# Performance work log

Hardware: AMD Instinct MI355X
Metric: run time of the kernel (lower is better)

The kernel has to match this reference:

```python
import jax, jax.numpy as jnp
import numpy as np

N_NODES = 100000
N_EDGES = 3200000
N_F = 128
HIDDEN = 128
N_PRED = 8
K_HOPS = 3
N_GRAPHS = 64


def setup_inputs() -> dict:
    key = jax.random.key(0)
    k1, k2, k3, k4, k5, k6, k7, k8 = jax.random.split(key, 8)
    x = jax.random.normal(k1, (N_NODES, N_F), dtype=jnp.float32)
    edge_index = jax.random.randint(k2, (2, N_EDGES), 0, N_NODES, dtype=jnp.int64)
    edge_attr = jax.random.uniform(k3, (N_EDGES,), dtype=jnp.float32)
    batch = jnp.sort(jax.random.randint(k4, (N_NODES,), 0, N_GRAPHS, dtype=jnp.int64))
    # SGConv internal Linear: in=n_f, out=hidden (applied after K propagations)
    s1 = 1.0 / np.sqrt(N_F)
    W_conv = jax.random.uniform(k5, (HIDDEN, N_F), dtype=jnp.float32, minval=-s1, maxval=s1)
    b_conv = jax.random.uniform(k6, (HIDDEN,), dtype=jnp.float32, minval=-s1, maxval=s1)
    s2 = 1.0 / np.sqrt(HIDDEN)
    W_lin = jax.random.uniform(k7, (N_PRED, HIDDEN), dtype=jnp.float32, minval=-s2, maxval=s2)
    b_lin = jax.random.uniform(k8, (N_PRED,), dtype=jnp.float32, minval=-s2, maxval=s2)
    return {"x": x, "edge_index": edge_index, "edge_attr": edge_attr, "batch": batch,
            "W_conv": W_conv, "b_conv": b_conv, "W_lin": W_lin, "b_lin": b_lin}


def _gcn_norm(edge_index, edge_weight, num_nodes):
    # Add self-loops with weight 1 (PyG gcn_norm default), then symmetric normalize.
    loop = jnp.arange(num_nodes, dtype=edge_index.dtype)
    row = jnp.concatenate([edge_index[0], loop])
    col = jnp.concatenate([edge_index[1], loop])
    w = jnp.concatenate([edge_weight, jnp.ones((num_nodes,), dtype=edge_weight.dtype)])
    deg = jax.ops.segment_sum(w, col, num_segments=num_nodes)
    dinv = jnp.where(deg > 0, jax.lax.rsqrt(jnp.where(deg > 0, deg, 1.0)), 0.0)
    norm = dinv[row] * w * dinv[col]
    return row, col, norm


def reference(x, edge_index, edge_attr, batch, W_conv, b_conv, W_lin, b_lin):
    N = x.shape[0]
    row, col, norm = _gcn_norm(edge_index, edge_attr, N)
    h = x
    for _ in range(K_HOPS):  # K repeated gather-scale-scatter propagations
        h = jax.ops.segment_sum(norm[:, None] * h[row], col, num_segments=N)
    h = h @ W_conv.T + b_conv  # SGConv linear: [N, hidden]
    # global_mean_pool by batch id
    sums = jax.ops.segment_sum(h, batch, num_segments=N_GRAPHS)
    cnt = jax.ops.segment_sum(jnp.ones((N,), dtype=h.dtype), batch, num_segments=N_GRAPHS)
    pooled = sums / jnp.maximum(cnt, 1.0)[:, None]
    # dropout(p=0.5) is identity in eval mode
    return pooled @ W_lin.T + b_lin
```

## Files before the change

kernel.cpp:

```cpp
#include <hip/hip_runtime.h>

#define NN 100000
#define NE 3200000
#define NF 128
#define NH 128
#define NP 8
#define NG 64

#define CS 16000
#define NC 7
#define NW 64
#define ES (NE / NW)

#define PT 64
#define GP 1024

#define SCAN_B 1024
#define SCAN_NBLK 98

__device__ __forceinline__ unsigned short f2bf(float f) {
    unsigned u = __float_as_uint(f);
    return (unsigned short)((u + 0x7fffu + ((u >> 16) & 1u)) >> 16);
}
__device__ __forceinline__ float bf2f(unsigned short b) {
    return __uint_as_float((unsigned)b << 16);
}

__global__ void k_init(float* __restrict__ cnt, float* __restrict__ psum) {
    int i = blockIdx.x * blockDim.x + threadIdx.x;
    if (i < NG) cnt[i] = 0.0f;
    if (i < NG * NH) psum[i] = 0.0f;
}

__global__ __launch_bounds__(256) void k_hist(const int* __restrict__ row,
                                              unsigned* __restrict__ H) {
    __shared__ unsigned hist[CS];
    int w = blockIdx.x % NW, c = blockIdx.x / NW;
    int rbase = c * CS;
    int nb = (rbase + CS <= NN) ? CS : (NN - rbase);
    for (int i = threadIdx.x; i < nb; i += 256) hist[i] = 0u;
    __syncthreads();
    const int4* r4 = (const int4*)(row + (size_t)w * ES);
    for (int i = threadIdx.x; i < ES / 8; i += 256) {
        int4 a = r4[2 * i], b = r4[2 * i + 1];
        int rs[8] = {a.x, a.y, a.z, a.w, b.x, b.y, b.z, b.w};
#pragma unroll
        for (int j = 0; j < 8; ++j) {
            unsigned rr = (unsigned)(rs[j] - rbase);
            if (rr < (unsigned)nb) atomicAdd(&hist[rr], 1u);
        }
    }
    __syncthreads();
    for (int i = threadIdx.x; i < nb; i += 256) H[(size_t)w * NN + rbase + i] = hist[i];
}

__global__ __launch_bounds__(256) void k_deg_hist(const int* __restrict__ col,
                                                  const float* __restrict__ wt,
                                                  float* __restrict__ Hd) {
    __shared__ float dh[CS];
    int w = blockIdx.x % NW, c = blockIdx.x / NW;
    int rbase = c * CS;
    int nb = (rbase + CS <= NN) ? CS : (NN - rbase);
    for (int i = threadIdx.x; i < nb; i += 256) dh[i] = 0.0f;
    __syncthreads();
    const int4*   c4 = (const int4*)(col + (size_t)w * ES);
    const float4* w4 = (const float4*)(wt + (size_t)w * ES);
    for (int i = threadIdx.x; i < ES / 8; i += 256) {
        int4 a = c4[2 * i], b = c4[2 * i + 1];
        float4 wa = w4[2 * i], wb = w4[2 * i + 1];
        int cc[8] = {a.x, a.y, a.z, a.w, b.x, b.y, b.z, b.w};
        float ww[8] = {wa.x, wa.y, wa.z, wa.w, wb.x, wb.y, wb.z, wb.w};
#pragma unroll
        for (int j = 0; j < 8; ++j) {
            unsigned rr = (unsigned)(cc[j] - rbase);
            if (rr < (unsigned)nb) atomicAdd(&dh[rr], ww[j]);
        }
    }
    __syncthreads();
    for (int i = threadIdx.x; i < nb; i += 256) Hd[(size_t)w * NN + rbase + i] = dh[i];
}

__global__ void k_cnt(const int* __restrict__ batch, float* __restrict__ cnt) {
    __shared__ float c[NG];
    int t = threadIdx.x;
    if (t < NG) c[t] = 0.0f;
    __syncthreads();
    int i = blockIdx.x * blockDim.x + t;
    if (i < NN) atomicAdd(&c[batch[i]], 1.0f);
    __syncthreads();
    if (t < NG && c[t] != 0.0f) atomicAdd(&cnt[t], c[t]);
}

__global__ void k_reduce(const unsigned* __restrict__ H, const float* __restrict__ Hd,
                         int* __restrict__ rcnt, float* __restrict__ dinv) {
    int r = blockIdx.x * blockDim.x + threadIdx.x;
    if (r >= NN) return;
    unsigned s = 0;
    float d = 1.0f;
#pragma unroll
    for (int w = 0; w < NW; ++w) {
        s += H[(size_t)w * NN + r];
        d += Hd[(size_t)w * NN + r];
    }
    rcnt[r] = (int)s;
    dinv[r] = rsqrtf(d);
}

__global__ __launch_bounds__(SCAN_B) void k_scan1(const int* __restrict__ rcnt,
                                                  int* __restrict__ px,
                                                  int* __restrict__ bsum) {
    __shared__ int s[SCAN_B];
    int t = threadIdx.x;
    int i = blockIdx.x * SCAN_B + t;
    int v = (i < NN) ? rcnt[i] : 0;
    s[t] = v;
    __syncthreads();
    for (int off = 1; off < SCAN_B; off <<= 1) {
        int x = (t >= off) ? s[t - off] : 0;
        __syncthreads();
        s[t] += x;
        __syncthreads();
    }
    px[i] = s[t] - v;
    if (t == SCAN_B - 1) bsum[blockIdx.x] = s[t];
}

__global__ void k_scan2(const int* __restrict__ bsum, int* __restrict__ bofs) {
    if (threadIdx.x == 0) {
        int acc = 0;
        for (int b = 0; b < SCAN_NBLK; ++b) { bofs[b] = acc; acc += bsum[b]; }
    }
}

__global__ void k_scan3(const int* __restrict__ px, const int* __restrict__ bofs,
                        int* __restrict__ rowptr) {
    int i = blockIdx.x * blockDim.x + threadIdx.x;
    if (i > NN) return;
    rowptr[i] = px[i] + bofs[i >> 10];
}

__global__ void k_base(const int* __restrict__ rowptr, unsigned* __restrict__ H) {
    int r = blockIdx.x * blockDim.x + threadIdx.x;
    if (r >= NN) return;
    unsigned acc = (unsigned)rowptr[r];
#pragma unroll
    for (int w = 0; w < NW; ++w) {
        unsigned v = H[(size_t)w * NN + r];
        H[(size_t)w * NN + r] = acc;
        acc += v;
    }
}

__global__ __launch_bounds__(256) void k_sort(const int* __restrict__ row,
                                              const int* __restrict__ col,
                                              const float* __restrict__ wt,
                                              const unsigned* __restrict__ B,
                                              const float* __restrict__ dinv,
                                              float2* __restrict__ pack) {
    __shared__ unsigned basel[CS];
    int w = blockIdx.x % NW, c = blockIdx.x / NW;
    int rbase = c * CS;
    int nb = (rbase + CS <= NN) ? CS : (NN - rbase);
    for (int i = threadIdx.x; i < nb; i += 256)
        basel[i] = B[(size_t)w * NN + rbase + i];
    __syncthreads();
    const int4*   r4 = (const int4*)(row + (size_t)w * ES);
    const int4*   c4 = (const int4*)(col + (size_t)w * ES);
    const float4* w4 = (const float4*)(wt + (size_t)w * ES);
    for (int i = threadIdx.x; i < ES / 8; i += 256) {
        int4 ra = r4[2 * i], rb = r4[2 * i + 1];
        int4 ca = c4[2 * i], cb = c4[2 * i + 1];
        float4 wa = w4[2 * i], wb = w4[2 * i + 1];
        int rs[8] = {ra.x, ra.y, ra.z, ra.w, rb.x, rb.y, rb.z, rb.w};
        int cs[8] = {ca.x, ca.y, ca.z, ca.w, cb.x, cb.y, cb.z, cb.w};
        float ww[8] = {wa.x, wa.y, wa.z, wa.w, wb.x, wb.y, wb.z, wb.w};
#pragma unroll
        for (int j = 0; j < 8; ++j) {
            unsigned rr = (unsigned)(rs[j] - rbase);
            if (rr < (unsigned)nb) {
                unsigned pos = atomicAdd(&basel[rr], 1u);
                pack[pos] = make_float2(__int_as_float(cs[j]),
                                        dinv[rs[j]] * ww[j] * dinv[cs[j]]);
            }
        }
    }
}

__global__ void k_q1_gather(const int* __restrict__ rowptr, const float2* __restrict__ pack,
                            const int* __restrict__ batch, const float* __restrict__ dinv,
                            unsigned short* __restrict__ Q) {
    int wid = (blockIdx.x * blockDim.x + threadIdx.x) >> 6;
    int lane = threadIdx.x & 63;
    if (wid >= NN) return;
    int beg = rowptr[wid], end = rowptr[wid + 1];
    float d = dinv[wid];
    float acc = (batch[wid] == lane) ? d * d : 0.0f;
    int e = beg;
    for (; e + 8 <= end; e += 8) {
        float2 p[8];
#pragma unroll
        for (int j = 0; j < 8; ++j) p[j] = pack[e + j];
        int b[8];
#pragma unroll
        for (int j = 0; j < 8; ++j) b[j] = batch[__float_as_int(p[j].x)];
#pragma unroll
        for (int j = 0; j < 8; ++j) acc += (b[j] == lane) ? p[j].y : 0.0f;
    }
    for (; e < end; ++e) {
        float2 p = pack[e];
        acc += (batch[__float_as_int(p.x)] == lane) ? p.y : 0.0f;
    }
    Q[(wid << 6) + lane] = f2bf(acc);
}

__global__ void k_hop_gather(const int* __restrict__ rowptr, const float2* __restrict__ pack,
                             const float* __restrict__ dinv,
                             const unsigned short* __restrict__ Qin,
                             unsigned short* __restrict__ Qout) {
    int wid = (blockIdx.x * blockDim.x + threadIdx.x) >> 6;
    int lane = threadIdx.x & 63;
    if (wid >= NN) return;
    int beg = rowptr[wid], end = rowptr[wid + 1];
    float d = dinv[wid];
    float acc = d * d * bf2f(Qin[(wid << 6) + lane]);
    int e = beg;
    for (; e + 8 <= end; e += 8) {
        float2 p[8];
#pragma unroll
        for (int j = 0; j < 8; ++j) p[j] = pack[e + j];
        unsigned short q[8];
#pragma unroll
        for (int j = 0; j < 8; ++j) q[j] = Qin[(__float_as_int(p[j].x) << 6) + lane];
#pragma unroll
        for (int j = 0; j < 8; ++j) acc += p[j].y * bf2f(q[j]);
    }
    for (; e < end; ++e) {
        float2 p = pack[e];
        acc += p.y * bf2f(Qin[(__float_as_int(p.x) << 6) + lane]);
    }
    Qout[(wid << 6) + lane] = f2bf(acc);
}

__global__ __launch_bounds__(256) void k_pool(const unsigned short* __restrict__ Q,
                                              const float* __restrict__ x,
                                              float* __restrict__ partial) {
    __shared__ unsigned short qsh[PT * NG];
    __shared__ float xs[PT * NF];
    int t = threadIdx.x;
    int f4 = (t & 31) << 2;
    int g0 = (t >> 5) << 3;
    float4 acc[8];
#pragma unroll
    for (int i = 0; i < 8; ++i) acc[i] = make_float4(0.f, 0.f, 0.f, 0.f);

    const int NT = (NN + PT - 1) / PT;
    for (int tile = blockIdx.x; tile < NT; tile += GP) {
        int n0 = tile * PT;
        int nt = min(PT, NN - n0);
        const uint4*  Q4 = (const uint4*)(Q + (size_t)n0 * NG);
        const float4* X4 = (const float4*)(x + (size_t)n0 * NF);
        uint4*  qs4 = (uint4*)qsh;
        float4* xs4 = (float4*)xs;
        for (int i = t; i < nt * (NG / 8); i += 256) qs4[i] = Q4[i];
        for (int i = t; i < nt * (NF / 4); i += 256) xs4[i] = X4[i];
        __syncthreads();
        for (int n = 0; n < nt; ++n) {
            float4 xv = *(const float4*)&xs[n * NF + f4];
            uint4 qu = *(const uint4*)&qsh[n * NG + g0];
            float qv[8];
            qv[0] = __uint_as_float(qu.x << 16);
            qv[1] = __uint_as_float(qu.x & 0xffff0000u);
            qv[2] = __uint_as_float(qu.y << 16);
            qv[3] = __uint_as_float(qu.y & 0xffff0000u);
            qv[4] = __uint_as_float(qu.z << 16);
            qv[5] = __uint_as_float(qu.z & 0xffff0000u);
            qv[6] = __uint_as_float(qu.w << 16);
            qv[7] = __uint_as_float(qu.w & 0xffff0000u);
#pragma unroll
            for (int i = 0; i < 8; ++i) {
                acc[i].x += qv[i] * xv.x;
                acc[i].y += qv[i] * xv.y;
                acc[i].z += qv[i] * xv.z;
                acc[i].w += qv[i] * xv.w;
            }
        }
        __syncthreads();
    }
    float* pb = partial + (size_t)blockIdx.x * (NG * NF);
#pragma unroll
    for (int i = 0; i < 8; ++i)
        *(float4*)&pb[(g0 + i) * NF + f4] = acc[i];
}

__global__ void k_red(const float* __restrict__ partial, float* __restrict__ psum) {
    int gid = blockIdx.x * blockDim.x + threadIdx.x;
    int idx = gid & (NG * NF - 1);
    int j = gid >> 13;
    float acc = 0.0f;
    for (int b = j; b < GP; b += 8)
        acc += partial[(size_t)b * (NG * NF) + idx];
    atomicAdd(&psum[idx], acc);
}

__global__ void k_final(const float* __restrict__ psum, const float* __restrict__ cnt,
                        const float* __restrict__ Wc, const float* __restrict__ bc,
                        const float* __restrict__ Wl, const float* __restrict__ bl,
                        float* __restrict__ out) {
    __shared__ float M[NP * NH];
    __shared__ float bias[NP];
    int t = threadIdx.x;
    for (int idx = t; idx < NP * NH; idx += 256) {
        int p = idx >> 7, f = idx & 127;
        float s = 0.0f;
        for (int h = 0; h < NH; ++h) s += Wl[p * NH + h] * Wc[h * NF + f];
        M[idx] = s;
    }
    if (t < NP) {
        float s = bl[t];
        for (int h = 0; h < NH; ++h) s += Wl[t * NH + h] * bc[h];
        bias[t] = s;
    }
    __syncthreads();
    for (int idx = t; idx < NG * NP; idx += 256) {
        int g = idx >> 3, p = idx & 7;
        float inv = 1.0f / fmaxf(cnt[g], 1.0f);
        float s = 0.0f;
        for (int f = 0; f < NF; ++f) s += psum[g * NF + f] * M[p * NH + f];
        out[idx] = s * inv + bias[p];
    }
}

extern "C" void kernel_launch(void* const* d_in, const int* in_sizes, int n_in,
                              void* d_out, int out_size, void* d_ws, size_t ws_size,
                              hipStream_t stream) {
    const float* x     = (const float*)d_in[0];
    const int*   ei    = (const int*)d_in[1];
    const float* ea    = (const float*)d_in[2];
    const int*   batch = (const int*)d_in[3];
    const float* Wc    = (const float*)d_in[4];
    const float* bc    = (const float*)d_in[5];
    const float* Wl    = (const float*)d_in[6];
    const float* bl    = (const float*)d_in[7];
    const int* row = ei;
    const int* col = ei + NE;
    float* out = (float*)d_out;

    float* ws     = (float*)d_ws;
    float*  dinv   = ws;
    int*    rowptr = (int*)(dinv + NN);
    float*  cnt    = (float*)(rowptr + NN + 4);
    float*  psum   = cnt + NG;
    float2* pack   = (float2*)(psum + NG * NH);
    unsigned* H    = (unsigned*)(pack + NE);
    float*    Hd   = (float*)(H + (size_t)NW * NN);
    unsigned short* Qa = (unsigned short*)H;
    unsigned short* Qb = Qa + (size_t)NN * NG;
    float* partial = (float*)Qb;
    int* rcnt = (int*)pack;
    int* px   = rcnt + SCAN_NBLK * SCAN_B;
    int* bsum = px + SCAN_NBLK * SCAN_B;
    int* bofs = bsum + SCAN_NBLK;

    const int B = 256;
    int gN  = (NN + B - 1) / B;
    int gCW = NC * NW;
    int gW  = (int)(((long long)NN * 64 + B - 1) / B);

    k_init<<<(NG * NH + B - 1) / B, B, 0, stream>>>(cnt, psum);
    k_hist<<<gCW, B, 0, stream>>>(row, H);
    k_deg_hist<<<gCW, B, 0, stream>>>(col, ea, Hd);
    k_cnt<<<gN, B, 0, stream>>>(batch, cnt);
    k_reduce<<<gN, B, 0, stream>>>(H, Hd, rcnt, dinv);

    k_scan1<<<SCAN_NBLK, SCAN_B, 0, stream>>>(rcnt, px, bsum);
    k_scan2<<<1, 64, 0, stream>>>(bsum, bofs);
    k_scan3<<<(NN + 1 + SCAN_B - 1) / SCAN_B, SCAN_B, 0, stream>>>(px, bofs, rowptr);
    k_base<<<gN, B, 0, stream>>>(rowptr, H);
    k_sort<<<gCW, B, 0, stream>>>(row, col, ea, H, dinv, pack);

    k_q1_gather<<<gW, B, 0, stream>>>(rowptr, pack, batch, dinv, Qa);
    k_hop_gather<<<gW, B, 0, stream>>>(rowptr, pack, dinv, Qa, Qb);
    k_hop_gather<<<gW, B, 0, stream>>>(rowptr, pack, dinv, Qb, Qa);

    k_pool<<<GP, B, 0, stream>>>(Qa, x, partial);
    k_red<<<256, B, 0, stream>>>(partial, psum);
    k_final<<<1, B, 0, stream>>>(psum, cnt, Wc, bc, Wl, bl, out);
}
```

Measured before the change: 681.4 us.

## Split Q into four 16-column slabs and process hop gather per slab

Stores the propagated graph-projection matrix Q as four contiguous slabs of 16 bf16 columns. Each hop-gather pass now touches only one 3.2 MB slab, so that pass's random-access working set can stay in cache. Each wave handles one node with four edge groups of 16 lanes, then combines them with cross-lane shuffles. The pack column index is pre-scaled into a byte offset and read with nontemporal loads to skip index arithmetic and avoid polluting the cache. In exchange, the edge list is re-read once per pass (four times instead of once), and the pool kernel's loads are rearranged to match the new layout.

```diff
diff --git a/kernel.cpp b/kernel.cpp
--- a/kernel.cpp
+++ b/kernel.cpp
@@ -14,6 +14,9 @@
 
 #define PT 64
 #define GP 1024
+
+#define NPASS 4
+#define HB 25000
 
 #define SCAN_B 1024
 #define SCAN_NBLK 98
@@ -179,7 +182,7 @@
             unsigned rr = (unsigned)(rs[j] - rbase);
             if (rr < (unsigned)nb) {
                 unsigned pos = atomicAdd(&basel[rr], 1u);
-                pack[pos] = make_float2(__int_as_float(cs[j]),
+                pack[pos] = make_float2(__int_as_float(cs[j] << 5),
                                         dinv[rs[j]] * ww[j] * dinv[cs[j]]);
             }
         }
@@ -195,60 +198,78 @@
     int beg = rowptr[wid], end = rowptr[wid + 1];
     float d = dinv[wid];
     float acc = (batch[wid] == lane) ? d * d : 0.0f;
+    const char* bc8 = (const char*)batch;
+    const unsigned long long* pk = (const unsigned long long*)pack;
     int e = beg;
     for (; e + 8 <= end; e += 8) {
-        float2 p[8];
-#pragma unroll
-        for (int j = 0; j < 8; ++j) p[j] = pack[e + j];
+        unsigned long long p[8];
+#pragma unroll
+        for (int j = 0; j < 8; ++j)
+            p[j] = __builtin_nontemporal_load(pk + e + j);
         int b[8];
 #pragma unroll
-        for (int j = 0; j < 8; ++j) b[j] = batch[__float_as_int(p[j].x)];
-#pragma unroll
-        for (int j = 0; j < 8; ++j) acc += (b[j] == lane) ? p[j].y : 0.0f;
+        for (int j = 0; j < 8; ++j)
+            b[j] = *(const int*)(bc8 + (((unsigned)p[j]) >> 3));
+#pragma unroll
+        for (int j = 0; j < 8; ++j)
+            acc += (b[j] == lane) ? __uint_as_float((unsigned)(p[j] >> 32)) : 0.0f;
     }
     for (; e < end; ++e) {
-        float2 p = pack[e];
-        acc += (batch[__float_as_int(p.x)] == lane) ? p.y : 0.0f;
-    }
-    Q[(wid << 6) + lane] = f2bf(acc);
+        unsigned long long p = pk[e];
+        acc += (*(const int*)(bc8 + (((unsigned)p) >> 3)) == lane)
+               ? __uint_as_float((unsigned)(p >> 32)) : 0.0f;
+    }
+    Q[(size_t)(lane >> 4) * (NN * 16) + wid * 16 + (lane & 15)] = f2bf(acc);
 }
 
 __global__ void k_hop_gather(const int* __restrict__ rowptr, const float2* __restrict__ pack,
                              const float* __restrict__ dinv,
                              const unsigned short* __restrict__ Qin,
                              unsigned short* __restrict__ Qout) {
-    int wid = (blockIdx.x * blockDim.x + threadIdx.x) >> 6;
+    int pass = blockIdx.x / HB;
+    int wid = (blockIdx.x % HB) * 4 + (threadIdx.x >> 6);
     int lane = threadIdx.x & 63;
-    if (wid >= NN) return;
+    int g = lane >> 4, j = lane & 15;
+    const char* qc = (const char*)(Qin + (size_t)pass * (NN * 16));
+    unsigned short* qo = Qout + (size_t)pass * (NN * 16);
+    const unsigned long long* pk = (const unsigned long long*)pack;
     int beg = rowptr[wid], end = rowptr[wid + 1];
-    float d = dinv[wid];
-    float acc = d * d * bf2f(Qin[(wid << 6) + lane]);
-    int e = beg;
-    for (; e + 8 <= end; e += 8) {
-        float2 p[8];
-#pragma unroll
-        for (int j = 0; j < 8; ++j) p[j] = pack[e + j];
-        unsigned short q[8];
-#pragma unroll
-        for (int j = 0; j < 8; ++j) q[j] = Qin[(__float_as_int(p[j].x) << 6) + lane];
-#pragma unroll
-        for (int j = 0; j < 8; ++j) acc += p[j].y * bf2f(q[j]);
-    }
-    for (; e < end; ++e) {
-        float2 p = pack[e];
-        acc += p.y * bf2f(Qin[(__float_as_int(p.x) << 6) + lane]);
-    }
-    Qout[(wid << 6) + lane] = f2bf(acc);
+    float acc = 0.0f;
+    if (g == 0) {
+        float d = dinv[wid];
+        acc = d * d * bf2f(*(const unsigned short*)(qc + wid * 32 + j * 2));
+    }
+    unsigned j2 = (unsigned)(j * 2);
+    int e = beg + g;
+    for (; e + 4 < end; e += 8) {
+        unsigned long long w0 = __builtin_nontemporal_load(pk + e);
+        unsigned long long w1 = __builtin_nontemporal_load(pk + e + 4);
+        unsigned short q0 = *(const unsigned short*)(qc + ((unsigned)w0 + j2));
+        unsigned short q1 = *(const unsigned short*)(qc + ((unsigned)w1 + j2));
+        acc += __uint_as_float((unsigned)(w0 >> 32)) * bf2f(q0);
+        acc += __uint_as_float((unsigned)(w1 >> 32)) * bf2f(q1);
+    }
+    for (; e < end; e += 4) {
+        unsigned long long w = __builtin_nontemporal_load(pk + e);
+        acc += __uint_as_float((unsigned)(w >> 32)) *
+               bf2f(*(const unsigned short*)(qc + ((unsigned)w + j2)));
+    }
+    acc += __shfl_xor(acc, 16);
+    acc += __shfl_xor(acc, 32);
+    if (g == 0)
+        __builtin_nontemporal_store(f2bf(acc), &qo[wid * 16 + j]);
 }
 
 __global__ __launch_bounds__(256) void k_pool(const unsigned short* __restrict__ Q,
                                               const float* __restrict__ x,
                                               float* __restrict__ partial) {
-    __shared__ unsigned short qsh[PT * NG];
+    __shared__ unsigned short qsh[NPASS * PT * 16];
     __shared__ float xs[PT * NF];
     int t = threadIdx.x;
     int f4 = (t & 31) << 2;
     int g0 = (t >> 5) << 3;
+    int qch = g0 >> 4;
+    int qof = g0 & 15;
     float4 acc[8];
 #pragma unroll
     for (int i = 0; i < 8; ++i) acc[i] = make_float4(0.f, 0.f, 0.f, 0.f);
@@ -257,16 +278,19 @@
     for (int tile = blockIdx.x; tile < NT; tile += GP) {
         int n0 = tile * PT;
         int nt = min(PT, NN - n0);
-        const uint4*  Q4 = (const uint4*)(Q + (size_t)n0 * NG);
         const float4* X4 = (const float4*)(x + (size_t)n0 * NF);
-        uint4*  qs4 = (uint4*)qsh;
         float4* xs4 = (float4*)xs;
-        for (int i = t; i < nt * (NG / 8); i += 256) qs4[i] = Q4[i];
+#pragma unroll
+        for (int c = 0; c < NPASS; ++c) {
+            const uint4* Qc = (const uint4*)(Q + (size_t)c * (NN * 16) + (size_t)n0 * 16);
+            uint4* qs4 = (uint4*)&qsh[c * PT * 16];
+            for (int i = t; i < nt * 2; i += 256) qs4[i] = Qc[i];
+        }
         for (int i = t; i < nt * (NF / 4); i += 256) xs4[i] = X4[i];
         __syncthreads();
         for (int n = 0; n < nt; ++n) {
             float4 xv = *(const float4*)&xs[n * NF + f4];
-            uint4 qu = *(const uint4*)&qsh[n * NG + g0];
+            uint4 qu = *(const uint4*)&qsh[qch * PT * 16 + n * 16 + qof];
             float qv[8];
             qv[0] = __uint_as_float(qu.x << 16);
             qv[1] = __uint_as_float(qu.x & 0xffff0000u);
@@ -379,8 +403,8 @@
     k_sort<<<gCW, B, 0, stream>>>(row, col, ea, H, dinv, pack);
 
     k_q1_gather<<<gW, B, 0, stream>>>(rowptr, pack, batch, dinv, Qa);
-    k_hop_gather<<<gW, B, 0, stream>>>(rowptr, pack, dinv, Qa, Qb);
-    k_hop_gather<<<gW, B, 0, stream>>>(rowptr, pack, dinv, Qb, Qa);
+    k_hop_gather<<<NPASS * HB, B, 0, stream>>>(rowptr, pack, dinv, Qa, Qb);
+    k_hop_gather<<<NPASS * HB, B, 0, stream>>>(rowptr, pack, dinv, Qb, Qa);
 
     k_pool<<<GP, B, 0, stream>>>(Qa, x, partial);
     k_red<<<256, B, 0, stream>>>(partial, psum);
```

After: 1.041 ms. +52.8%, slower.
